# Performance work log

Measured on AMD Instinct MI355X. Metric: run time of the kernel, lower is better.

The kernel has to match this reference:

```python
import jax, jax.numpy as jnp
import numpy as np

N_T = 8
N_R = 2
NOISE = 1e-12  # 10**(-120/10)
B = 65536


def setup_inputs() -> dict:
    key = jax.random.key(0)
    ks = jax.random.split(key, 7)
    return {
        "theta1": jax.random.normal(ks[0], (B, 264), dtype=jnp.float32),
        "G1r": jax.random.normal(ks[1], (B, N_R, 100), dtype=jnp.float32),
        "G1i": jax.random.normal(ks[2], (B, N_R, 100), dtype=jnp.float32),
        "G2r": jax.random.normal(ks[3], (B, N_R, 100), dtype=jnp.float32),
        "G2i": jax.random.normal(ks[4], (B, N_R, 100), dtype=jnp.float32),
        "Ur": jax.random.normal(ks[5], (B, 100, N_T), dtype=jnp.float32),
        "Ui": jax.random.normal(ks[6], (B, 100, N_T), dtype=jnp.float32),
    }


def _rate(phi, Fsig, Fintf):
    # phi: [B, N_r, N_t], Fsig/Fintf: [B, N_t, N_r]
    A = jnp.einsum("bnt,btr->bnr", phi, Fsig)    # signal term  [B, N_r, N_r]
    C = jnp.einsum("bnt,btr->bnr", phi, Fintf)   # interference [B, N_r, N_r]
    # Mu = C C^H + noise (elementwise scalar add, faithful to torch source)
    Mu = jnp.einsum("bnr,bmr->bnm", C, jnp.conj(C)) + NOISE
    inner = jnp.einsum("brn,bnm,bms->brs", jnp.conj(A).transpose(0, 2, 1) if False else jnp.conj(jnp.swapaxes(A, 1, 2)), jnp.linalg.inv(Mu), A)
    # note: torch does 1 + matrix (elementwise), not identity add
    return jnp.real(jnp.log(jnp.linalg.det(1.0 + inner)))  # [B]


def reference(theta1, G1r, G1i, G2r, G2i, Ur, Ui):
    M1N1 = N_T * N_R  # 16
    F1 = theta1[:, 200:200 + M1N1] + 1j * theta1[:, 200 + M1N1:200 + 2 * M1N1]
    F2 = theta1[:, 200 + 2 * M1N1:200 + 3 * M1N1] + 1j * theta1[:, 200 + 3 * M1N1:]
    # power normalization: F * sqrt(2 / (F^H F))
    F1 = F1 * jnp.sqrt(2.0 / jnp.sum(jnp.conj(F1) * F1, axis=1, keepdims=True))
    F2 = F2 * jnp.sqrt(2.0 / jnp.sum(jnp.conj(F2) * F2, axis=1, keepdims=True))
    F1m = F1.reshape(-1, N_T, N_R)
    F2m = F2.reshape(-1, N_T, N_R)

    theta = theta1[:, 0:100] + 1j * theta1[:, 100:200]  # [B, 100]
    G1 = G1r + 1j * G1i
    G2 = G2r + 1j * G2i
    U = Ur + 1j * Ui

    # phi = G @ diag(theta) @ U, vectorized over batch
    phi1 = jnp.einsum("bnk,bk,bkt->bnt", G1, theta, U)  # [B, N_r, N_t]
    phi2 = jnp.einsum("bnk,bk,bkt->bnt", G2, theta, U)

    R1 = _rate(phi1, F1m, F2m)
    R2 = _rate(phi2, F2m, F1m)
    R = jnp.maximum(-R1, -R2)
    return jnp.sum(R) / theta1.shape[0]
```

## Files before the change

kernel.cpp:

```cpp
#include <hip/hip_runtime.h>
#include <math.h>

#define NOISE 1e-12f
#define WSZ 1064
#define WSZ4 266

typedef float f32x2 __attribute__((ext_vector_type(2)));

__device__ __forceinline__ f32x2 mk2(float x, float y){ f32x2 r; r.x = x; r.y = y; return r; }

__device__ __forceinline__ f32x2 cmul_pk(f32x2 a, f32x2 b) {
    f32x2 w;
    asm("v_pk_mul_f32 %0, %1, %2 op_sel:[0,0] op_sel_hi:[0,1]\n\t"
        "v_pk_fma_f32 %0, %1, %2, %0 op_sel:[1,1,0] op_sel_hi:[1,0,1] neg_lo:[0,1,0]"
        : "=&v"(w) : "v"(a), "v"(b));
    return w;
}
__device__ __forceinline__ void cfma_pk(f32x2& p, f32x2 a, f32x2 w) {
    asm("v_pk_fma_f32 %0, %1, %2, %0 op_sel:[0,0,0] op_sel_hi:[0,1,1]\n\t"
        "v_pk_fma_f32 %0, %1, %2, %0 op_sel:[1,1,0] op_sel_hi:[1,0,1] neg_lo:[0,1,0]"
        : "+v"(p) : "v"(a), "v"(w));
}

__device__ __forceinline__ float2 cmul(float2 a, float2 b) {
    return make_float2(a.x*b.x - a.y*b.y, a.x*b.y + a.y*b.x);
}
__device__ __forceinline__ float2 cconjmul(float2 a, float2 b) {
    return make_float2(a.x*b.x + a.y*b.y, a.x*b.y - a.y*b.x);
}
__device__ __forceinline__ float2 cmulconj(float2 a, float2 b) {
    return make_float2(a.x*b.x + a.y*b.y, a.y*b.x - a.x*b.y);
}
__device__ __forceinline__ float2 cadd(float2 a, float2 b){ return make_float2(a.x+b.x, a.y+b.y); }
__device__ __forceinline__ float2 csub(float2 a, float2 b){ return make_float2(a.x-b.x, a.y-b.y); }
__device__ __forceinline__ float2 cscale(float s, float2 a){ return make_float2(s*a.x, s*a.y); }

typedef const void __attribute__((address_space(1)))* gas_t;
typedef void __attribute__((address_space(3)))* las_t;
__device__ __forceinline__ void gll4(const float* g, float* l) {
    __builtin_amdgcn_global_load_lds((gas_t)g, (las_t)l, 4, 0, 0);
}

__global__ __launch_bounds__(256) void rate_kernel(
    const float* __restrict__ t1,
    const float* __restrict__ G1r, const float* __restrict__ G1i,
    const float* __restrict__ G2r, const float* __restrict__ G2i,
    const float* __restrict__ Ur,  const float* __restrict__ Ui,
    float* __restrict__ partial)
{
    __shared__ float4 lds4[4 * WSZ4];
    __shared__ float2 ent[4][4][16];
    __shared__ float wsum[4];
    const int wave = threadIdx.x >> 6;
    const int lane = threadIdx.x & 63;
    const int t2 = lane & 3;
    const int k0 = lane >> 2;
    float* W = (float*)(lds4 + wave * WSZ4);

    const int half  = lane & 1;
    const int qh    = lane >> 1;

    #define STAGE(dst, bb) {                                                   \
        const float* tb_ = t1 + (long)(bb) * 264;                              \
        const float* ts  = tb_ + (half ? 100 : 0) + qh;                        \
        gll4(ts,       (dst));        gll4(ts + 32,  (dst) + 64);              \
        gll4(ts + 64,  (dst) + 128);                                           \
        if (lane < 8) gll4(ts + 96, (dst) + 192);                              \
        gll4(tb_ + 200 + lane, (dst) + 200);                                   \
        const float* g1 = (half ? G1i : G1r) + (long)(bb) * 200 + qh;          \
        const float* g2 = (half ? G2i : G2r) + (long)(bb) * 200 + qh;          \
        gll4(g1,        (dst)+264);   gll4(g1+32,  (dst)+328);                 \
        gll4(g1+64,     (dst)+392);   gll4(g1+96,  (dst)+456);                 \
        gll4(g1+128,    (dst)+520);   gll4(g1+160, (dst)+584);                 \
        if (lane < 16) gll4(g1+192, (dst)+648);                                \
        gll4(g2,        (dst)+664);   gll4(g2+32,  (dst)+728);                 \
        gll4(g2+64,     (dst)+792);   gll4(g2+96,  (dst)+856);                 \
        gll4(g2+128,    (dst)+920);   gll4(g2+160, (dst)+984);                 \
        if (lane < 16) gll4(g2+192, (dst)+1048);                               \
    }

    const long bbase = (long)blockIdx.x * 16 + (long)wave * 4;
    STAGE(W, bbase);

    const float* urb = Ur + bbase * 800;
    const float* uib = Ui + bbase * 800;
    const int ubase = 8 * k0 + 2 * t2;
    const int utail = 8 * (96 + (k0 < 4 ? k0 : 3)) + 2 * t2;
    #define LD2(p, idx) (*(const float2*)((p) + (idx)))

    float2 g0r = LD2(urb, ubase),       g0i = LD2(uib, ubase);
    float2 g1r = LD2(urb, ubase+128),   g1i = LD2(uib, ubase+128);
    float2 g2r = LD2(urb, ubase+256),   g2i = LD2(uib, ubase+256);
    float2 g3r = LD2(urb, ubase+384),   g3i = LD2(uib, ubase+384);

    #define JBODY(j, gr, gi) {                                        \
        const int kk = 2*k0 + 32*(j);                                 \
        f32x2 th = *(const f32x2*)(W + kk);                           \
        f32x2 ga = *(const f32x2*)(W + 264 + kk);                     \
        f32x2 gc = *(const f32x2*)(W + 464 + kk);                     \
        f32x2 gd = *(const f32x2*)(W + 664 + kk);                     \
        f32x2 ge = *(const f32x2*)(W + 864 + kk);                     \
        f32x2 w0 = cmul_pk(th, mk2((gr).x, (gi).x));                  \
        f32x2 w1 = cmul_pk(th, mk2((gr).y, (gi).y));                  \
        cfma_pk(p10a, ga, w0);  cfma_pk(p10b, ga, w1);                \
        cfma_pk(p11a, gc, w0);  cfma_pk(p11b, gc, w1);                \
        cfma_pk(p20a, gd, w0);  cfma_pk(p20b, gd, w1);                \
        cfma_pk(p21a, ge, w0);  cfma_pk(p21b, ge, w1); }

    const int idxF = lane & 15;
    const int selF = (lane >> 4) & 1;
    const bool useF1 = (k0 < 4) || (k0 >= 12);
    const int fb = useF1 ? 200 : 232;
    const int i0 = 4*t2 + (k0 & 1);

    #pragma unroll 1
    for (int it = 0; it < 4; ++it) {
        asm volatile("s_waitcnt vmcnt(8)" ::: "memory");
        __builtin_amdgcn_sched_barrier(0);

        float fr = W[200 + selF*32 + idxF];
        float fi = W[216 + selF*32 + idxF];
        float2 fv0 = make_float2(W[fb + i0],     W[fb + 16 + i0]);
        float2 fv1 = make_float2(W[fb + i0 + 2], W[fb + 18 + i0]);

        f32x2 p10a=mk2(0,0), p10b=mk2(0,0), p11a=mk2(0,0), p11b=mk2(0,0);
        f32x2 p20a=mk2(0,0), p20b=mk2(0,0), p21a=mk2(0,0), p21b=mk2(0,0);

        float2 g4r = LD2(urb, ubase+512), g4i = LD2(uib, ubase+512);
        JBODY(0, g0r, g0i);
        float2 g5r = LD2(urb, ubase+640), g5i = LD2(uib, ubase+640);
        JBODY(1, g1r, g1i);
        float2 g6r = LD2(urb, utail),     g6i = LD2(uib, utail);
        JBODY(2, g2r, g2i);
        JBODY(3, g3r, g3i);
        JBODY(4, g4r, g4i);
        JBODY(5, g5r, g5i);
        if (k0 < 4) JBODY(6, g6r, g6i);

        if (it < 3) {
            asm volatile("s_waitcnt lgkmcnt(0)" ::: "memory");
            __builtin_amdgcn_sched_barrier(0);
            STAGE(W, bbase + it + 1);
            __builtin_amdgcn_sched_barrier(0);
            urb += 800; uib += 800;
            g0r = LD2(urb, ubase);     g0i = LD2(uib, ubase);
            g1r = LD2(urb, ubase+128); g1i = LD2(uib, ubase+128);
            g2r = LD2(urb, ubase+256); g2i = LD2(uib, ubase+256);
            g3r = LD2(urb, ubase+384); g3i = LD2(uib, ubase+384);
            __builtin_amdgcn_sched_barrier(0);
        }

        float q[16] = {p10a.x,p10a.y,p10b.x,p10b.y,
                       p11a.x,p11a.y,p11b.x,p11b.y,
                       p20a.x,p20a.y,p20b.x,p20b.y,
                       p21a.x,p21a.y,p21b.x,p21b.y};
        #pragma unroll
        for (int i = 0; i < 16; ++i) q[i] += __shfl_xor(q[i], 4);
        const int nsel = (lane >> 3) & 1;
        float r8[8];
        #pragma unroll
        for (int i = 0; i < 4; ++i) {
            float ka = nsel ? q[4+i]  : q[i];
            float sa = nsel ? q[i]    : q[4+i];
            r8[i]   = ka + __shfl_xor(sa, 8);
            float kb = nsel ? q[12+i] : q[8+i];
            float sb = nsel ? q[8+i]  : q[12+i];
            r8[4+i] = kb + __shfl_xor(sb, 8);
        }
        #pragma unroll
        for (int i = 0; i < 8; ++i) r8[i] += __shfl_xor(r8[i], 16);
        const int msel = (lane >> 5) & 1;
        float ph[4];
        #pragma unroll
        for (int i = 0; i < 4; ++i) {
            float kp = msel ? r8[4+i] : r8[i];
            float sp = msel ? r8[i]   : r8[4+i];
            ph[i] = kp + __shfl_xor(sp, 32);
        }

        float m = fr*fr + fi*fi;
        #pragma unroll
        for (int s = 1; s < 16; s <<= 1) m += __shfl_xor(m, s);
        float other = __shfl_xor(m, 16);
        float nrm1 = selF ? other : m;
        float nrm2 = selF ? m : other;
        float sc1 = sqrtf(2.0f / nrm1);
        float sc2 = sqrtf(2.0f / nrm2);
        float sE = useF1 ? sc1 : sc2;

        float2 E = cadd(cmul(make_float2(ph[0], ph[1]), fv0),
                        cmul(make_float2(ph[2], ph[3]), fv1));
        E.x += __shfl_xor(E.x, 1); E.y += __shfl_xor(E.y, 1);
        E.x += __shfl_xor(E.x, 2); E.y += __shfl_xor(E.y, 2);
        if (t2 == 0) ent[wave][it][k0] = cscale(sE, E);
    }
    #undef STAGE
    #undef LD2
    #undef JBODY
    asm volatile("s_waitcnt lgkmcnt(0)" ::: "memory");
    __builtin_amdgcn_wave_barrier();

    float negR = 0.0f;
    if (lane < 8) {
        const float2* e = &ent[wave][lane >> 1][(lane & 1) * 8];
        float2 A00=e[0], A01=e[1], A10=e[2], A11=e[3];
        float2 C00=e[4], C01=e[5], C10=e[6], C11=e[7];
        float mu00 = C00.x*C00.x + C00.y*C00.y + C01.x*C01.x + C01.y*C01.y + NOISE;
        float mu11 = C10.x*C10.x + C10.y*C10.y + C11.x*C11.x + C11.y*C11.y + NOISE;
        float2 mu01 = cadd(cmulconj(C00, C10), cmulconj(C01, C11));
        mu01.x += NOISE;
        float det = mu00*mu11 - (mu01.x*mu01.x + mu01.y*mu01.y);
        float inv = 1.0f / det;
        float2 mu01c = make_float2(mu01.x, -mu01.y);
        float2 X00 = cscale(inv, csub(cscale(mu11, A00), cmul(mu01,  A10)));
        float2 X01 = cscale(inv, csub(cscale(mu11, A01), cmul(mu01,  A11)));
        float2 X10 = cscale(inv, csub(cscale(mu00, A10), cmul(mu01c, A00)));
        float2 X11 = cscale(inv, csub(cscale(mu00, A11), cmul(mu01c, A01)));
        float2 I00 = cadd(cconjmul(A00, X00), cconjmul(A10, X10));
        float2 I01 = cadd(cconjmul(A00, X01), cconjmul(A10, X11));
        float2 I10 = cadd(cconjmul(A01, X00), cconjmul(A11, X10));
        float2 I11 = cadd(cconjmul(A01, X01), cconjmul(A11, X11));
        I00.x += 1.0f; I01.x += 1.0f; I10.x += 1.0f; I11.x += 1.0f;
        float2 dT = csub(cmul(I00, I11), cmul(I01, I10));
        negR = -0.5f * logf(dT.x*dT.x + dT.y*dT.y);
    }
    float m = fmaxf(negR, __shfl_xor(negR, 1));
    m += __shfl_xor(m, 2);
    m += __shfl_xor(m, 4);
    if (lane == 0) wsum[wave] = m;

    __syncthreads();
    if (threadIdx.x == 0)
        partial[blockIdx.x] = (wsum[0] + wsum[1]) + (wsum[2] + wsum[3]);
}

__global__ __launch_bounds__(256) void reduce_kernel(
    const float* __restrict__ partial, int n, float invB, float* __restrict__ out)
{
    __shared__ float sd[256];
    float s = 0.0f;
    for (int i = threadIdx.x; i < n; i += 256) s += partial[i];
    sd[threadIdx.x] = s;
    __syncthreads();
    for (int o = 128; o > 0; o >>= 1) {
        if ((int)threadIdx.x < o) sd[threadIdx.x] += sd[threadIdx.x + o];
        __syncthreads();
    }
    if (threadIdx.x == 0) out[0] = sd[0] * invB;
}

extern "C" void kernel_launch(void* const* d_in, const int* in_sizes, int n_in,
                              void* d_out, int out_size, void* d_ws, size_t ws_size,
                              hipStream_t stream) {
    const float* t1  = (const float*)d_in[0];
    const float* G1r = (const float*)d_in[1];
    const float* G1i = (const float*)d_in[2];
    const float* G2r = (const float*)d_in[3];
    const float* G2i = (const float*)d_in[4];
    const float* Ur  = (const float*)d_in[5];
    const float* Ui  = (const float*)d_in[6];

    const int B = in_sizes[0] / 264;
    const int nblocks = B / 16;
    float* partial = (float*)d_ws;

    rate_kernel<<<nblocks, 256, 0, stream>>>(t1, G1r, G1i, G2r, G2i, Ur, Ui, partial);
    reduce_kernel<<<1, 256, 0, stream>>>(partial, nblocks, 1.0f / (float)B, (float*)d_out);
}
```

Before: 135.0 us.

## Widen LDS staging to 16-byte loads and regroup lanes for float4 U reads

Replaces the many 4-byte global_load_lds operations with 16-byte ones that copy theta and the G rows contiguously into LDS. It also remaps lanes so each lane handles a k index and a half of the t columns, reading U with float4 loads. This cuts the number of memory instructions and the vmcnt depth, and reworks the cross-lane reduction tree to match. In exchange each lane holds more accumulators, which raises register pressure, and the planar LDS layout may cause bank conflicts on scalar LDS reads.

```diff
diff --git a/kernel.cpp b/kernel.cpp
--- a/kernel.cpp
+++ b/kernel.cpp
@@ -37,8 +37,8 @@
 
 typedef const void __attribute__((address_space(1)))* gas_t;
 typedef void __attribute__((address_space(3)))* las_t;
-__device__ __forceinline__ void gll4(const float* g, float* l) {
-    __builtin_amdgcn_global_load_lds((gas_t)g, (las_t)l, 4, 0, 0);
+__device__ __forceinline__ void gll16(const float* g, float* l) {
+    __builtin_amdgcn_global_load_lds((gas_t)g, (las_t)l, 16, 0, 0);
 }
 
 __global__ __launch_bounds__(256) void rate_kernel(
@@ -53,30 +53,20 @@
     __shared__ float wsum[4];
     const int wave = threadIdx.x >> 6;
     const int lane = threadIdx.x & 63;
-    const int t2 = lane & 3;
-    const int k0 = lane >> 2;
+    const int h  = lane & 1;
+    const int k0 = lane >> 1;
     float* W = (float*)(lds4 + wave * WSZ4);
-
-    const int half  = lane & 1;
-    const int qh    = lane >> 1;
 
     #define STAGE(dst, bb) {                                                   \
         const float* tb_ = t1 + (long)(bb) * 264;                              \
-        const float* ts  = tb_ + (half ? 100 : 0) + qh;                        \
-        gll4(ts,       (dst));        gll4(ts + 32,  (dst) + 64);              \
-        gll4(ts + 64,  (dst) + 128);                                           \
-        if (lane < 8) gll4(ts + 96, (dst) + 192);                              \
-        gll4(tb_ + 200 + lane, (dst) + 200);                                   \
-        const float* g1 = (half ? G1i : G1r) + (long)(bb) * 200 + qh;          \
-        const float* g2 = (half ? G2i : G2r) + (long)(bb) * 200 + qh;          \
-        gll4(g1,        (dst)+264);   gll4(g1+32,  (dst)+328);                 \
-        gll4(g1+64,     (dst)+392);   gll4(g1+96,  (dst)+456);                 \
-        gll4(g1+128,    (dst)+520);   gll4(g1+160, (dst)+584);                 \
-        if (lane < 16) gll4(g1+192, (dst)+648);                                \
-        gll4(g2,        (dst)+664);   gll4(g2+32,  (dst)+728);                 \
-        gll4(g2+64,     (dst)+792);   gll4(g2+96,  (dst)+856);                 \
-        gll4(g2+128,    (dst)+920);   gll4(g2+160, (dst)+984);                 \
-        if (lane < 16) gll4(g2+192, (dst)+1048);                               \
+        gll16(tb_ + lane * 4, (dst));                                          \
+        if (lane < 2)  gll16(tb_ + 256 + lane * 4, (dst) + 256);               \
+        if (lane < 50) {                                                       \
+            gll16(G1r + (long)(bb) * 200 + lane * 4, (dst) + 264);             \
+            gll16(G1i + (long)(bb) * 200 + lane * 4, (dst) + 464);             \
+            gll16(G2r + (long)(bb) * 200 + lane * 4, (dst) + 664);             \
+            gll16(G2i + (long)(bb) * 200 + lane * 4, (dst) + 864);             \
+        }                                                                      \
     }
 
     const long bbase = (long)blockIdx.x * 16 + (long)wave * 4;
@@ -84,58 +74,58 @@
 
     const float* urb = Ur + bbase * 800;
     const float* uib = Ui + bbase * 800;
-    const int ubase = 8 * k0 + 2 * t2;
-    const int utail = 8 * (96 + (k0 < 4 ? k0 : 3)) + 2 * t2;
-    #define LD2(p, idx) (*(const float2*)((p) + (idx)))
-
-    float2 g0r = LD2(urb, ubase),       g0i = LD2(uib, ubase);
-    float2 g1r = LD2(urb, ubase+128),   g1i = LD2(uib, ubase+128);
-    float2 g2r = LD2(urb, ubase+256),   g2i = LD2(uib, ubase+256);
-    float2 g3r = LD2(urb, ubase+384),   g3i = LD2(uib, ubase+384);
-
-    #define JBODY(j, gr, gi) {                                        \
-        const int kk = 2*k0 + 32*(j);                                 \
-        f32x2 th = *(const f32x2*)(W + kk);                           \
-        f32x2 ga = *(const f32x2*)(W + 264 + kk);                     \
-        f32x2 gc = *(const f32x2*)(W + 464 + kk);                     \
-        f32x2 gd = *(const f32x2*)(W + 664 + kk);                     \
-        f32x2 ge = *(const f32x2*)(W + 864 + kk);                     \
-        f32x2 w0 = cmul_pk(th, mk2((gr).x, (gi).x));                  \
-        f32x2 w1 = cmul_pk(th, mk2((gr).y, (gi).y));                  \
-        cfma_pk(p10a, ga, w0);  cfma_pk(p10b, ga, w1);                \
-        cfma_pk(p11a, gc, w0);  cfma_pk(p11b, gc, w1);                \
-        cfma_pk(p20a, gd, w0);  cfma_pk(p20b, gd, w1);                \
-        cfma_pk(p21a, ge, w0);  cfma_pk(p21b, ge, w1); }
+    const int ubase = 8 * k0 + 4 * h;
+    const int utail = 768 + 8 * (k0 < 4 ? k0 : 3) + 4 * h;
+    #define LD4(p, idx) (*(const float4*)((p) + (idx)))
+
+    float4 u0r = LD4(urb, ubase),     u0i = LD4(uib, ubase);
+    float4 u1r = LD4(urb, ubase+256), u1i = LD4(uib, ubase+256);
+
+    #define JBODY(kk, ur4, ui4) {                                     \
+        f32x2 th = mk2(W[(kk)],     W[100+(kk)]);                     \
+        f32x2 ga = mk2(W[264+(kk)], W[464+(kk)]);                     \
+        f32x2 gc = mk2(W[364+(kk)], W[564+(kk)]);                     \
+        f32x2 gd = mk2(W[664+(kk)], W[864+(kk)]);                     \
+        f32x2 ge = mk2(W[764+(kk)], W[964+(kk)]);                     \
+        f32x2 w0 = cmul_pk(th, mk2((ur4).x,(ui4).x));                 \
+        f32x2 w1 = cmul_pk(th, mk2((ur4).y,(ui4).y));                 \
+        f32x2 w2 = cmul_pk(th, mk2((ur4).z,(ui4).z));                 \
+        f32x2 w3 = cmul_pk(th, mk2((ur4).w,(ui4).w));                 \
+        cfma_pk(pa0,ga,w0); cfma_pk(pa1,ga,w1); cfma_pk(pa2,ga,w2); cfma_pk(pa3,ga,w3); \
+        cfma_pk(pb0,gc,w0); cfma_pk(pb1,gc,w1); cfma_pk(pb2,gc,w2); cfma_pk(pb3,gc,w3); \
+        cfma_pk(pc0,gd,w0); cfma_pk(pc1,gd,w1); cfma_pk(pc2,gd,w2); cfma_pk(pc3,gd,w3); \
+        cfma_pk(pd0,ge,w0); cfma_pk(pd1,ge,w1); cfma_pk(pd2,ge,w2); cfma_pk(pd3,ge,w3); }
 
     const int idxF = lane & 15;
     const int selF = (lane >> 4) & 1;
-    const bool useF1 = (k0 < 4) || (k0 >= 12);
+    const int rF   = (lane >> 2) & 1;
+    const bool useF1 = (((lane >> 4) & 1) == ((lane >> 5) & 1));
     const int fb = useF1 ? 200 : 232;
-    const int i0 = 4*t2 + (k0 & 1);
+    const int fi0 = 8 * h + rF;
 
     #pragma unroll 1
     for (int it = 0; it < 4; ++it) {
-        asm volatile("s_waitcnt vmcnt(8)" ::: "memory");
+        asm volatile("s_waitcnt vmcnt(4)" ::: "memory");
         __builtin_amdgcn_sched_barrier(0);
 
-        float fr = W[200 + selF*32 + idxF];
-        float fi = W[216 + selF*32 + idxF];
-        float2 fv0 = make_float2(W[fb + i0],     W[fb + 16 + i0]);
-        float2 fv1 = make_float2(W[fb + i0 + 2], W[fb + 18 + i0]);
-
-        f32x2 p10a=mk2(0,0), p10b=mk2(0,0), p11a=mk2(0,0), p11b=mk2(0,0);
-        f32x2 p20a=mk2(0,0), p20b=mk2(0,0), p21a=mk2(0,0), p21b=mk2(0,0);
-
-        float2 g4r = LD2(urb, ubase+512), g4i = LD2(uib, ubase+512);
-        JBODY(0, g0r, g0i);
-        float2 g5r = LD2(urb, ubase+640), g5i = LD2(uib, ubase+640);
-        JBODY(1, g1r, g1i);
-        float2 g6r = LD2(urb, utail),     g6i = LD2(uib, utail);
-        JBODY(2, g2r, g2i);
-        JBODY(3, g3r, g3i);
-        JBODY(4, g4r, g4i);
-        JBODY(5, g5r, g5i);
-        if (k0 < 4) JBODY(6, g6r, g6i);
+        float fnr = W[200 + selF*32 + idxF];
+        float fni = W[216 + selF*32 + idxF];
+        float2 fv0 = make_float2(W[fb + fi0],     W[fb + 16 + fi0]);
+        float2 fv1 = make_float2(W[fb + fi0 + 2], W[fb + 18 + fi0]);
+        float2 fv2 = make_float2(W[fb + fi0 + 4], W[fb + 20 + fi0]);
+        float2 fv3 = make_float2(W[fb + fi0 + 6], W[fb + 22 + fi0]);
+
+        f32x2 pa0=mk2(0,0),pa1=mk2(0,0),pa2=mk2(0,0),pa3=mk2(0,0);
+        f32x2 pb0=mk2(0,0),pb1=mk2(0,0),pb2=mk2(0,0),pb3=mk2(0,0);
+        f32x2 pc0=mk2(0,0),pc1=mk2(0,0),pc2=mk2(0,0),pc3=mk2(0,0);
+        f32x2 pd0=mk2(0,0),pd1=mk2(0,0),pd2=mk2(0,0),pd3=mk2(0,0);
+
+        float4 u2r = LD4(urb, ubase+512), u2i = LD4(uib, ubase+512);
+        JBODY(k0, u0r, u0i);
+        float4 utr = LD4(urb, utail),     uti = LD4(uib, utail);
+        JBODY(k0+32, u1r, u1i);
+        JBODY(k0+64, u2r, u2i);
+        if (k0 < 4) JBODY(k0+96, utr, uti);
 
         if (it < 3) {
             asm volatile("s_waitcnt lgkmcnt(0)" ::: "memory");
@@ -143,42 +133,40 @@
             STAGE(W, bbase + it + 1);
             __builtin_amdgcn_sched_barrier(0);
             urb += 800; uib += 800;
-            g0r = LD2(urb, ubase);     g0i = LD2(uib, ubase);
-            g1r = LD2(urb, ubase+128); g1i = LD2(uib, ubase+128);
-            g2r = LD2(urb, ubase+256); g2i = LD2(uib, ubase+256);
-            g3r = LD2(urb, ubase+384); g3i = LD2(uib, ubase+384);
+            u0r = LD4(urb, ubase);     u0i = LD4(uib, ubase);
+            u1r = LD4(urb, ubase+256); u1i = LD4(uib, ubase+256);
             __builtin_amdgcn_sched_barrier(0);
         }
 
-        float q[16] = {p10a.x,p10a.y,p10b.x,p10b.y,
-                       p11a.x,p11a.y,p11b.x,p11b.y,
-                       p20a.x,p20a.y,p20b.x,p20b.y,
-                       p21a.x,p21a.y,p21b.x,p21b.y};
-        #pragma unroll
-        for (int i = 0; i < 16; ++i) q[i] += __shfl_xor(q[i], 4);
+        float q[32] = {pa0.x,pa0.y,pa1.x,pa1.y,pa2.x,pa2.y,pa3.x,pa3.y,
+                       pb0.x,pb0.y,pb1.x,pb1.y,pb2.x,pb2.y,pb3.x,pb3.y,
+                       pc0.x,pc0.y,pc1.x,pc1.y,pc2.x,pc2.y,pc3.x,pc3.y,
+                       pd0.x,pd0.y,pd1.x,pd1.y,pd2.x,pd2.y,pd3.x,pd3.y};
+        const int msel = (lane >> 5) & 1;
+        float r16[16];
+        #pragma unroll
+        for (int i = 0; i < 16; ++i) {
+            float ka = msel ? q[16+i] : q[i];
+            float sa = msel ? q[i]    : q[16+i];
+            r16[i] = ka + __shfl_xor(sa, 32);
+        }
+        #pragma unroll
+        for (int i = 0; i < 16; ++i) r16[i] += __shfl_xor(r16[i], 16);
         const int nsel = (lane >> 3) & 1;
         float r8[8];
         #pragma unroll
-        for (int i = 0; i < 4; ++i) {
-            float ka = nsel ? q[4+i]  : q[i];
-            float sa = nsel ? q[i]    : q[4+i];
-            r8[i]   = ka + __shfl_xor(sa, 8);
-            float kb = nsel ? q[12+i] : q[8+i];
-            float sb = nsel ? q[8+i]  : q[12+i];
-            r8[4+i] = kb + __shfl_xor(sb, 8);
-        }
-        #pragma unroll
-        for (int i = 0; i < 8; ++i) r8[i] += __shfl_xor(r8[i], 16);
-        const int msel = (lane >> 5) & 1;
-        float ph[4];
-        #pragma unroll
-        for (int i = 0; i < 4; ++i) {
-            float kp = msel ? r8[4+i] : r8[i];
-            float sp = msel ? r8[i]   : r8[4+i];
-            ph[i] = kp + __shfl_xor(sp, 32);
-        }
-
-        float m = fr*fr + fi*fi;
+        for (int i = 0; i < 8; ++i) {
+            float ka = nsel ? r16[8+i] : r16[i];
+            float sa = nsel ? r16[i]   : r16[8+i];
+            r8[i] = ka + __shfl_xor(sa, 8);
+        }
+        #pragma unroll
+        for (int i = 0; i < 8; ++i) {
+            r8[i] += __shfl_xor(r8[i], 4);
+            r8[i] += __shfl_xor(r8[i], 2);
+        }
+
+        float m = fnr*fnr + fni*fni;
         #pragma unroll
         for (int s = 1; s < 16; s <<= 1) m += __shfl_xor(m, s);
         float other = __shfl_xor(m, 16);
@@ -188,14 +176,15 @@
         float sc2 = sqrtf(2.0f / nrm2);
         float sE = useF1 ? sc1 : sc2;
 
-        float2 E = cadd(cmul(make_float2(ph[0], ph[1]), fv0),
-                        cmul(make_float2(ph[2], ph[3]), fv1));
+        float2 E = cadd(cadd(cmul(make_float2(r8[0],r8[1]), fv0),
+                             cmul(make_float2(r8[2],r8[3]), fv1)),
+                        cadd(cmul(make_float2(r8[4],r8[5]), fv2),
+                             cmul(make_float2(r8[6],r8[7]), fv3)));
         E.x += __shfl_xor(E.x, 1); E.y += __shfl_xor(E.y, 1);
-        E.x += __shfl_xor(E.x, 2); E.y += __shfl_xor(E.y, 2);
-        if (t2 == 0) ent[wave][it][k0] = cscale(sE, E);
+        if ((lane & 3) == 0) ent[wave][it][lane >> 2] = cscale(sE, E);
     }
     #undef STAGE
-    #undef LD2
+    #undef LD4
     #undef JBODY
     asm volatile("s_waitcnt lgkmcnt(0)" ::: "memory");
     __builtin_amdgcn_wave_barrier();
```

Result: no change. 134.3 us (-0.5%).
